# Optimization experiments

Hardware: AMD Instinct MI355X
Metric: run time of the kernel (lower is better)

The kernel has to match this reference:

```python
import jax, jax.numpy as jnp
import numpy as np

EPS = 1e-5  # BatchNorm eps
N_NODES, N_EDGES, F = 100000, 600000, 128


def setup_inputs() -> dict:
    key = jax.random.key(0)
    ks = jax.random.split(key, 16)
    inp = {
        "node_representations": jax.random.normal(ks[0], (N_NODES, F), jnp.float32),
        "edges": jax.random.randint(ks[1], (2, N_EDGES), 0, N_NODES, jnp.int64 if jax.config.jax_enable_x64 else jnp.int32),
        "edge_weights": jax.random.uniform(ks[2], (N_EDGES,), jnp.float32),
        # preprocess FFN: BatchNorm1d(F) [eval mode] + Linear(F, F) + GELU
        "pre_bn_gamma": jax.random.normal(ks[3], (F,), jnp.float32) * 0.1 + 1.0,
        "pre_bn_beta": jax.random.normal(ks[4], (F,), jnp.float32) * 0.1,
        "pre_bn_mean": jax.random.normal(ks[5], (F,), jnp.float32) * 0.1,
        "pre_bn_var": jax.random.uniform(ks[6], (F,), jnp.float32) * 0.5 + 0.5,
        "pre_w": jax.random.normal(ks[7], (F, F), jnp.float32) / np.sqrt(F),
        "pre_b": jnp.zeros((F,), jnp.float32),
        # update FFN: BatchNorm1d(2F) [eval mode] + Linear(2F, F) + GELU
        "upd_bn_gamma": jax.random.normal(ks[8], (2 * F,), jnp.float32) * 0.1 + 1.0,
        "upd_bn_beta": jax.random.normal(ks[9], (2 * F,), jnp.float32) * 0.1,
        "upd_bn_mean": jax.random.normal(ks[10], (2 * F,), jnp.float32) * 0.1,
        "upd_bn_var": jax.random.uniform(ks[11], (2 * F,), jnp.float32) * 0.5 + 0.5,
        "upd_w": jax.random.normal(ks[12], (2 * F, F), jnp.float32) / np.sqrt(2 * F),
        "upd_b": jnp.zeros((F,), jnp.float32),
    }
    return inp


def _bn_eval(x, gamma, beta, mean, var):
    return (x - mean) * (gamma / jnp.sqrt(var + EPS)) + beta


def reference(node_representations, edges, edge_weights,
              pre_bn_gamma, pre_bn_beta, pre_bn_mean, pre_bn_var, pre_w, pre_b,
              upd_bn_gamma, upd_bn_beta, upd_bn_mean, upd_bn_var, upd_w, upd_b):
    n_nodes, f = node_representations.shape
    node_idx, nbr_idx = edges[0], edges[1]
    # gather neighbour features: [E, F]
    x = node_representations[nbr_idx]
    # preprocess FFN (BN eval, dropout=identity in eval, linear, gelu)
    x = _bn_eval(x, pre_bn_gamma, pre_bn_beta, pre_bn_mean, pre_bn_var)
    x = jax.nn.gelu(x @ pre_w + pre_b, approximate=False)
    x = x * edge_weights[:, None]
    # mean aggregation (replicates torch.unique-on-expanded-indices counter = degree * F)
    agg = jax.ops.segment_sum(x, node_idx, num_segments=n_nodes)
    deg = jax.ops.segment_sum(jnp.ones_like(edge_weights), node_idx, num_segments=n_nodes)
    counter = (deg * f)[:, None]
    agg = jnp.where(counter > 0, agg / jnp.where(counter > 0, counter, 1.0), 0.0)
    # concat combine + update FFN
    emb = jnp.concatenate([node_representations, agg], axis=-1)
    emb = _bn_eval(emb, upd_bn_gamma, upd_bn_beta, upd_bn_mean, upd_bn_var)
    emb = jax.nn.gelu(emb @ upd_w + upd_b, approximate=False)
    return emb
```

## Files before the change

kernel.cpp:

```cpp
#include <hip/hip_runtime.h>
#include <math.h>

#define F 128
#define TWO_F 256
#define BN_EPS 1e-5f
#define PAD_W2 264

typedef unsigned short ushort_t;
typedef unsigned char uchar_t;
typedef __attribute__((ext_vector_type(8))) short bfrag;
typedef __attribute__((ext_vector_type(4))) float ffrag;
typedef __attribute__((ext_vector_type(2))) float floatx2;

__device__ __forceinline__ float gelu_exact(float x) {
    return 0.5f * x * (1.0f + erff(x * 0.70710678118654752f));
}
__device__ __forceinline__ ushort_t f2bf(float x) {
    unsigned int u = __float_as_uint(x);
    u = (u + 0x7FFFu + ((u >> 16) & 1u)) >> 16;
    return (ushort_t)u;
}
__device__ __forceinline__ unsigned int pk2(float a, float b) {
    return (unsigned int)f2bf(a) | ((unsigned int)f2bf(b) << 16);
}

__device__ __forceinline__ void fma4_fp8(float* acc, unsigned int d, float w) {
    floatx2 lo = __builtin_amdgcn_cvt_pk_f32_fp8(d, false);
    floatx2 hi = __builtin_amdgcn_cvt_pk_f32_fp8(d, true);
    acc[0] = fmaf(w, lo.x, acc[0]);
    acc[1] = fmaf(w, lo.y, acc[1]);
    acc[2] = fmaf(w, hi.x, acc[2]);
    acc[3] = fmaf(w, hi.y, acc[3]);
}
__device__ __forceinline__ void fma16_fp8(float* acc, uint4 a, float w) {
    fma4_fp8(acc + 0,  a.x, w); fma4_fp8(acc + 4,  a.y, w);
    fma4_fp8(acc + 8,  a.z, w); fma4_fp8(acc + 12, a.w, w);
}

__device__ __forceinline__ bfrag pack8(float4 f0, float4 f1) {
    bfrag a;
    unsigned int* au = reinterpret_cast<unsigned int*>(&a);
    au[0] = pk2(f0.x, f0.y); au[1] = pk2(f0.z, f0.w);
    au[2] = pk2(f1.x, f1.y); au[3] = pk2(f1.z, f1.w);
    return a;
}

__global__ __launch_bounds__(256) void fold_hist(
    const float* __restrict__ pre_w, const float* __restrict__ pre_b,
    const float* __restrict__ g1, const float* __restrict__ be1,
    const float* __restrict__ m1, const float* __restrict__ v1,
    const float* __restrict__ upd_w, const float* __restrict__ upd_b,
    const float* __restrict__ g2, const float* __restrict__ be2,
    const float* __restrict__ m2, const float* __restrict__ v2,
    ushort_t* __restrict__ W1T, ushort_t* __restrict__ W2T,
    float* __restrict__ b1f, float* __restrict__ b2f,
    const int* __restrict__ edges, int* __restrict__ counts,
    int* __restrict__ rankb, int nEdges, int histBlocks) {
    const int t = threadIdx.x;
    if (blockIdx.x == 0) {
        __shared__ float t1[F], t2[TWO_F];
        if (t < F) {
            float s = g1[t] * rsqrtf(v1[t] + BN_EPS);
            t1[t] = be1[t] - m1[t] * s;
        }
        {
            float s = g2[t] * rsqrtf(v2[t] + BN_EPS);
            t2[t] = be2[t] - m2[t] * s;
        }
        __syncthreads();
        if (t < F) {
            float acc = pre_b[t];
            #pragma unroll 16
            for (int k = 0; k < F; ++k) acc = fmaf(t1[k], pre_w[k * F + t], acc);
            b1f[t] = acc;
        } else {
            int j = t - F;
            float acc = upd_b[j];
            #pragma unroll 16
            for (int k = 0; k < TWO_F; ++k) acc = fmaf(t2[k], upd_w[k * F + j], acc);
            b2f[j] = acc;
        }
    } else if (blockIdx.x <= 128) {
        int idx = (blockIdx.x - 1) * 256 + t;
        if (idx < F * F) {
            int k = idx & (F - 1), n = idx >> 7;
            float s = g1[k] * rsqrtf(v1[k] + BN_EPS);
            W1T[idx] = f2bf(s * pre_w[k * F + n]);
        }
        {
            int k = idx & (TWO_F - 1), n = idx >> 8;
            float s = g2[k] * rsqrtf(v2[k] + BN_EPS);
            W2T[idx] = f2bf(s * upd_w[k * F + n]);
        }
    } else {
        int b = blockIdx.x - 129;
        for (int i = b * 256 + t; i < nEdges; i += histBlocks * 256) {
            int rk = atomicAdd(&counts[edges[i]], 1);
            rankb[i] = rk;
        }
    }
}

__global__ __launch_bounds__(1024) void scan_pass1(const int* __restrict__ counts,
                                                   int* __restrict__ offsets,
                                                   int* __restrict__ blocksums, int n) {
    __shared__ int sb[1024];
    const int t = threadIdx.x;
    int idx = blockIdx.x * 1024 + t;
    int v = (idx < n) ? counts[idx] : 0;
    sb[t] = v;
    __syncthreads();
    for (int off = 1; off < 1024; off <<= 1) {
        int x = (t >= off) ? sb[t - off] : 0;
        __syncthreads();
        sb[t] += x;
        __syncthreads();
    }
    if (idx < n) offsets[idx + 1] = sb[t];
    if (t == 1023) blocksums[blockIdx.x] = sb[t];
}

__global__ __launch_bounds__(1024) void scan_pass3(const int* __restrict__ counts,
                                                   int* __restrict__ offsets,
                                                   const int* __restrict__ blocksums,
                                                   int* __restrict__ cursor, int n) {
    __shared__ int sb[1024];
    const int t = threadIdx.x;
    sb[t] = (t < blockIdx.x) ? blocksums[t] : 0;
    __syncthreads();
    #pragma unroll
    for (int off = 512; off > 0; off >>= 1) {
        if (t < off) sb[t] += sb[t + off];
        __syncthreads();
    }
    int base = sb[0];
    int idx = blockIdx.x * 1024 + t;
    if (idx < n) {
        int incl = offsets[idx + 1] + base;
        offsets[idx + 1] = incl;
        cursor[idx] = incl - counts[idx];
    }
    if (blockIdx.x == 0 && t == 0) offsets[0] = 0;
}

__global__ __launch_bounds__(256) void gemm1_fill(
    const float* __restrict__ nodes, const ushort_t* __restrict__ W1T,
    const float* __restrict__ b1f, uchar_t* __restrict__ G8, int nNodes,
    const int* __restrict__ edges, const float* __restrict__ ew,
    const int* __restrict__ offsets, const int* __restrict__ rankb,
    int2* __restrict__ csr, int nEdges, int gemmBlocks, int fillBlocks) {
    const int t = threadIdx.x;

    if (blockIdx.x >= gemmBlocks) {
        int b = blockIdx.x - gemmBlocks;
        for (int e = b * 256 + t; e < nEdges; e += fillBlocks * 256) {
            int dst = edges[e];
            int pos = offsets[dst] + rankb[e];
            csr[pos] = make_int2(edges[nEdges + e], __float_as_int(ew[e]));
        }
        return;
    }

    const int lane = t & 63, w = t >> 6;
    const int m = lane & 15, quad = lane >> 4;
    const int fw = w * 32;

    bfrag wf[2][4];
    #pragma unroll
    for (int cb = 0; cb < 2; ++cb)
        #pragma unroll
        for (int kk = 0; kk < 4; ++kk)
            wf[cb][kk] = *reinterpret_cast<const bfrag*>(
                W1T + (size_t)(fw + cb * 16 + m) * F + kk * 32 + quad * 8);

    float4 bias[2];
    #pragma unroll
    for (int cb = 0; cb < 2; ++cb)
        bias[cb] = *reinterpret_cast<const float4*>(b1f + fw + cb * 16 + quad * 4);

    const int tb = blockIdx.x * 256;

    #pragma unroll 2
    for (int g = 0; g < 16; ++g) {
        const int node = tb + g * 16 + m;
        const int sn = (node < nNodes) ? node : 0;
        const float* np = nodes + (size_t)sn * F + quad * 8;

        bfrag nf[4];
        #pragma unroll
        for (int kk = 0; kk < 4; ++kk) {
            float4 f0 = *reinterpret_cast<const float4*>(np + kk * 32);
            float4 f1 = *reinterpret_cast<const float4*>(np + kk * 32 + 4);
            nf[kk] = pack8(f0, f1);
        }

        ffrag acc[2];
        acc[0] = (ffrag){0.f, 0.f, 0.f, 0.f};
        acc[1] = (ffrag){0.f, 0.f, 0.f, 0.f};
        #pragma unroll
        for (int kk = 0; kk < 4; ++kk) {
            acc[0] = __builtin_amdgcn_mfma_f32_16x16x32_bf16(wf[0][kk], nf[kk], acc[0], 0, 0, 0);
            acc[1] = __builtin_amdgcn_mfma_f32_16x16x32_bf16(wf[1][kk], nf[kk], acc[1], 0, 0, 0);
        }

        if (node < nNodes) {
            #pragma unroll
            for (int cb = 0; cb < 2; ++cb) {
                float v0 = gelu_exact(acc[cb][0] + bias[cb].x);
                float v1 = gelu_exact(acc[cb][1] + bias[cb].y);
                float v2 = gelu_exact(acc[cb][2] + bias[cb].z);
                float v3 = gelu_exact(acc[cb][3] + bias[cb].w);
                int pw = __builtin_amdgcn_cvt_pk_fp8_f32(v0, v1, 0, false);
                pw = __builtin_amdgcn_cvt_pk_fp8_f32(v2, v3, pw, true);
                *reinterpret_cast<unsigned int*>(
                    G8 + (size_t)node * F + fw + cb * 16 + quad * 4) = (unsigned int)pw;
            }
        }
    }
}

__global__ __launch_bounds__(256) void gather_agg(
    const uchar_t* __restrict__ G8, const int* __restrict__ offsets,
    const int2* __restrict__ csr, ushort_t* __restrict__ agg, int nNodes) {
    const int t = threadIdx.x;
    const int gid = blockIdx.x * 32 + (t >> 3);
    const int q = t & 7;
    if (gid >= nNodes) return;
    const int s = offsets[gid], e = offsets[gid + 1];

    float acc[16];
    #pragma unroll
    for (int j = 0; j < 16; ++j) acc[j] = 0.f;

    int i = s;
    while (i < e) {
        int c = e - i;
        c = (c > 8) ? 8 : c;
        uint4 av[8];
        float wv[8];
        #pragma unroll
        for (int j = 0; j < 8; ++j) {
            if (j < c) {
                int2 m = csr[i + j];
                wv[j] = __int_as_float(m.y);
                av[j] = *reinterpret_cast<const uint4*>(
                    G8 + (size_t)(unsigned int)m.x * F + q * 16);
            }
        }
        #pragma unroll
        for (int j = 0; j < 8; ++j)
            if (j < c) fma16_fp8(acc, av[j], wv[j]);
        i += c;
    }

    const int deg = e - s;
    const float inv = (deg > 0) ? 1.0f / ((float)deg * (float)F) : 0.f;
    uint4 pv0, pv1;
    pv0.x = pk2(acc[0] * inv, acc[1] * inv);  pv0.y = pk2(acc[2] * inv, acc[3] * inv);
    pv0.z = pk2(acc[4] * inv, acc[5] * inv);  pv0.w = pk2(acc[6] * inv, acc[7] * inv);
    pv1.x = pk2(acc[8] * inv, acc[9] * inv);  pv1.y = pk2(acc[10] * inv, acc[11] * inv);
    pv1.z = pk2(acc[12] * inv, acc[13] * inv); pv1.w = pk2(acc[14] * inv, acc[15] * inv);
    uint4* d = reinterpret_cast<uint4*>(agg + (size_t)gid * F + q * 16);
    d[0] = pv0; d[1] = pv1;
}

__global__ __launch_bounds__(512, 4) void gemm2(
    const float* __restrict__ nodes, const ushort_t* __restrict__ agg,
    const ushort_t* __restrict__ W2T, const float* __restrict__ b2f,
    float* __restrict__ out, int nNodes) {
    __shared__ ushort_t Wl[F * PAD_W2];
    __shared__ float bsm[F];
    const int t = threadIdx.x;

    for (int j = t; j < 4096; j += 512) {
        int feat = j >> 5, kc = j & 31;
        *reinterpret_cast<uint4*>(Wl + feat * PAD_W2 + kc * 8) =
            reinterpret_cast<const uint4*>(W2T)[j];
    }
    if (t < F) bsm[t] = b2f[t];
    __syncthreads();

    const int lane = t & 63, w = t >> 6;
    const int m = lane & 15, quad = lane >> 4;
    const int tb = blockIdx.x * 256;

    int row0 = tb + w * 32 + m;
    int row1 = row0 + 16;
    int r0c = (row0 < nNodes) ? row0 : 0;
    int r1c = (row1 < nNodes) ? row1 : 0;
    const float*    p0n = nodes + (size_t)r0c * F + quad * 8;
    const float*    p1n = nodes + (size_t)r1c * F + quad * 8;
    const ushort_t* p0a = agg   + (size_t)r0c * F + quad * 8;
    const ushort_t* p1a = agg   + (size_t)r1c * F + quad * 8;

    ffrag acc0[8], acc1[8];
    #pragma unroll
    for (int c = 0; c < 8; ++c) {
        acc0[c] = (ffrag){0.f, 0.f, 0.f, 0.f};
        acc1[c] = (ffrag){0.f, 0.f, 0.f, 0.f};
    }

    #pragma unroll
    for (int kk = 0; kk < 8; ++kk) {
        int k0 = kk * 32 + quad * 8;
        bfrag a0, a1;
        if (kk < 4) {
            float4 f0 = *reinterpret_cast<const float4*>(p0n + kk * 32);
            float4 f1 = *reinterpret_cast<const float4*>(p0n + kk * 32 + 4);
            a0 = pack8(f0, f1);
            float4 g0 = *reinterpret_cast<const float4*>(p1n + kk * 32);
            float4 g1 = *reinterpret_cast<const float4*>(p1n + kk * 32 + 4);
            a1 = pack8(g0, g1);
        } else {
            a0 = *reinterpret_cast<const bfrag*>(p0a + (kk - 4) * 32);
            a1 = *reinterpret_cast<const bfrag*>(p1a + (kk - 4) * 32);
        }
        #pragma unroll
        for (int c = 0; c < 8; ++c) {
            bfrag b = *reinterpret_cast<const bfrag*>(Wl + (c * 16 + m) * PAD_W2 + k0);
            acc0[c] = __builtin_amdgcn_mfma_f32_16x16x32_bf16(a0, b, acc0[c], 0, 0, 0);
            acc1[c] = __builtin_amdgcn_mfma_f32_16x16x32_bf16(a1, b, acc1[c], 0, 0, 0);
        }
    }

    #pragma unroll
    for (int c = 0; c < 8; ++c) {
        int feat = c * 16 + m;
        float bj = bsm[feat];
        #pragma unroll
        for (int i = 0; i < 4; ++i) {
            int n0 = tb + w * 32 + quad * 4 + i;
            if (n0 < nNodes) out[(size_t)n0 * F + feat] = gelu_exact(acc0[c][i] + bj);
            int n1 = n0 + 16;
            if (n1 < nNodes) out[(size_t)n1 * F + feat] = gelu_exact(acc1[c][i] + bj);
        }
    }
}

extern "C" void kernel_launch(void* const* d_in, const int* in_sizes, int n_in,
                              void* d_out, int out_size, void* d_ws, size_t ws_size,
                              hipStream_t stream) {
    const float* nodes  = (const float*)d_in[0];
    const int*   edges  = (const int*)d_in[1];
    const float* ew     = (const float*)d_in[2];
    const float* pre_g  = (const float*)d_in[3];
    const float* pre_be = (const float*)d_in[4];
    const float* pre_m  = (const float*)d_in[5];
    const float* pre_v  = (const float*)d_in[6];
    const float* pre_w  = (const float*)d_in[7];
    const float* pre_b  = (const float*)d_in[8];
    const float* upd_g  = (const float*)d_in[9];
    const float* upd_be = (const float*)d_in[10];
    const float* upd_m  = (const float*)d_in[11];
    const float* upd_v  = (const float*)d_in[12];
    const float* upd_w  = (const float*)d_in[13];
    const float* upd_b  = (const float*)d_in[14];
    float* out = (float*)d_out;

    const int nNodes = in_sizes[0] / F;
    const int nEdges = in_sizes[2];
    const int nChunks = (nNodes + 1023) / 1024;
    const int histBlocks = 1024;
    const int fillBlocks = 512;
    const int gemmBlocks = (nNodes + 255) / 256;

    char* p = (char*)d_ws;
    int*      counts    = (int*)p;       p += (size_t)nNodes * 4;
    int*      offsets   = (int*)p;       p += (size_t)(nNodes + 4) * 4;
    int*      cursor    = (int*)p;       p += (size_t)nNodes * 4;
    int*      blocksums = (int*)p;       p += 1024 * 4;
    int2*     csr       = (int2*)p;      p += (size_t)nEdges * 8;
    float*    b1f       = (float*)p;     p += F * 4;
    float*    b2f       = (float*)p;     p += F * 4;
    ushort_t* W1T       = (ushort_t*)p;  p += F * F * 2;
    ushort_t* W2T       = (ushort_t*)p;  p += TWO_F * F * 2;
    uchar_t*  G8        = (uchar_t*)p;   p += (size_t)nNodes * F;
    ushort_t* agg       = (ushort_t*)p;  p += (size_t)nNodes * F * 2;
    int*      rankb     = (int*)p;

    hipMemsetAsync(counts, 0, (size_t)nNodes * 4, stream);

    fold_hist<<<129 + histBlocks, 256, 0, stream>>>(
        pre_w, pre_b, pre_g, pre_be, pre_m, pre_v,
        upd_w, upd_b, upd_g, upd_be, upd_m, upd_v,
        W1T, W2T, b1f, b2f, edges, counts, rankb, nEdges, histBlocks);

    scan_pass1<<<nChunks, 1024, 0, stream>>>(counts, offsets, blocksums, nNodes);
    scan_pass3<<<nChunks, 1024, 0, stream>>>(counts, offsets, blocksums, cursor, nNodes);

    gemm1_fill<<<gemmBlocks + fillBlocks, 256, 0, stream>>>(
        nodes, W1T, b1f, G8, nNodes, edges, ew, offsets, rankb, csr, nEdges,
        gemmBlocks, fillBlocks);

    gather_agg<<<(nNodes + 31) / 32, 256, 0, stream>>>(
        G8, offsets, csr, agg, nNodes);

    gemm2<<<(nNodes + 255) / 256, 512, 0, stream>>>(
        nodes, agg, W2T, b2f, out, nNodes);
}
```

Baseline: 267.9 us.

## Stage GEMM1 weights in LDS with persistent tiles and vectorize GEMM2 stores

GEMM1 now stages the bf16 weight matrix and bias in shared memory and loops persistently over 64-node tiles. Each wave computes all 128 output features for 16 nodes, so node rows are loaded once per wave and each wave writes full output rows. GEMM2 is restructured so each wave handles 16 nodes across all features and writes float4-vectorized output rows instead of scattered scalar stores. The 4-block occupancy hint on GEMM2 is dropped and its grid uses 128-node blocks. The trade is extra LDS traffic, since weights are reread from shared memory per tile, and higher register use from 8 accumulators.

```diff
diff --git a/kernel.cpp b/kernel.cpp
--- a/kernel.cpp
+++ b/kernel.cpp
@@ -4,6 +4,7 @@
 #define F 128
 #define TWO_F 256
 #define BN_EPS 1e-5f
+#define PAD_W1 136
 #define PAD_W2 264
 
 typedef unsigned short ushort_t;
@@ -148,7 +149,9 @@
     const float* __restrict__ b1f, uchar_t* __restrict__ G8, int nNodes,
     const int* __restrict__ edges, const float* __restrict__ ew,
     const int* __restrict__ offsets, const int* __restrict__ rankb,
-    int2* __restrict__ csr, int nEdges, int gemmBlocks, int fillBlocks) {
+    int2* __restrict__ csr, int nEdges, int gemmBlocks, int fillBlocks, int nTiles) {
+    __shared__ ushort_t Wl[F * PAD_W1];
+    __shared__ float bsm[F];
     const int t = threadIdx.x;
 
     if (blockIdx.x >= gemmBlocks) {
@@ -161,28 +164,19 @@
         return;
     }
 
+    for (int j = t; j < 2048; j += 256) {
+        int feat = j >> 4, kc = j & 15;
+        *reinterpret_cast<uint4*>(Wl + feat * PAD_W1 + kc * 8) =
+            reinterpret_cast<const uint4*>(W1T)[j];
+    }
+    if (t < F) bsm[t] = b1f[t];
+    __syncthreads();
+
     const int lane = t & 63, w = t >> 6;
     const int m = lane & 15, quad = lane >> 4;
-    const int fw = w * 32;
-
-    bfrag wf[2][4];
-    #pragma unroll
-    for (int cb = 0; cb < 2; ++cb)
-        #pragma unroll
-        for (int kk = 0; kk < 4; ++kk)
-            wf[cb][kk] = *reinterpret_cast<const bfrag*>(
-                W1T + (size_t)(fw + cb * 16 + m) * F + kk * 32 + quad * 8);
-
-    float4 bias[2];
-    #pragma unroll
-    for (int cb = 0; cb < 2; ++cb)
-        bias[cb] = *reinterpret_cast<const float4*>(b1f + fw + cb * 16 + quad * 4);
-
-    const int tb = blockIdx.x * 256;
-
-    #pragma unroll 2
-    for (int g = 0; g < 16; ++g) {
-        const int node = tb + g * 16 + m;
+
+    for (int tile = blockIdx.x; tile < nTiles; tile += gemmBlocks) {
+        const int node = tile * 64 + w * 16 + m;
         const int sn = (node < nNodes) ? node : 0;
         const float* np = nodes + (size_t)sn * F + quad * 8;
 
@@ -194,26 +188,32 @@
             nf[kk] = pack8(f0, f1);
         }
 
-        ffrag acc[2];
-        acc[0] = (ffrag){0.f, 0.f, 0.f, 0.f};
-        acc[1] = (ffrag){0.f, 0.f, 0.f, 0.f};
+        ffrag acc[8];
+        #pragma unroll
+        for (int cb = 0; cb < 8; ++cb) acc[cb] = (ffrag){0.f, 0.f, 0.f, 0.f};
+
         #pragma unroll
         for (int kk = 0; kk < 4; ++kk) {
-            acc[0] = __builtin_amdgcn_mfma_f32_16x16x32_bf16(wf[0][kk], nf[kk], acc[0], 0, 0, 0);
-            acc[1] = __builtin_amdgcn_mfma_f32_16x16x32_bf16(wf[1][kk], nf[kk], acc[1], 0, 0, 0);
+            int ko = kk * 32 + quad * 8;
+            #pragma unroll
+            for (int cb = 0; cb < 8; ++cb) {
+                bfrag a = *reinterpret_cast<const bfrag*>(Wl + (cb * 16 + m) * PAD_W1 + ko);
+                acc[cb] = __builtin_amdgcn_mfma_f32_16x16x32_bf16(a, nf[kk], acc[cb], 0, 0, 0);
+            }
         }
 
         if (node < nNodes) {
             #pragma unroll
-            for (int cb = 0; cb < 2; ++cb) {
-                float v0 = gelu_exact(acc[cb][0] + bias[cb].x);
-                float v1 = gelu_exact(acc[cb][1] + bias[cb].y);
-                float v2 = gelu_exact(acc[cb][2] + bias[cb].z);
-                float v3 = gelu_exact(acc[cb][3] + bias[cb].w);
+            for (int cb = 0; cb < 8; ++cb) {
+                float4 bj = *reinterpret_cast<const float4*>(bsm + cb * 16 + quad * 4);
+                float v0 = gelu_exact(acc[cb][0] + bj.x);
+                float v1 = gelu_exact(acc[cb][1] + bj.y);
+                float v2 = gelu_exact(acc[cb][2] + bj.z);
+                float v3 = gelu_exact(acc[cb][3] + bj.w);
                 int pw = __builtin_amdgcn_cvt_pk_fp8_f32(v0, v1, 0, false);
                 pw = __builtin_amdgcn_cvt_pk_fp8_f32(v2, v3, pw, true);
                 *reinterpret_cast<unsigned int*>(
-                    G8 + (size_t)node * F + fw + cb * 16 + quad * 4) = (unsigned int)pw;
+                    G8 + (size_t)node * F + cb * 16 + quad * 4) = (unsigned int)pw;
             }
         }
     }
@@ -264,7 +264,7 @@
     d[0] = pv0; d[1] = pv1;
 }
 
-__global__ __launch_bounds__(512, 4) void gemm2(
+__global__ __launch_bounds__(512) void gemm2(
     const float* __restrict__ nodes, const ushort_t* __restrict__ agg,
     const ushort_t* __restrict__ W2T, const float* __restrict__ b2f,
     float* __restrict__ out, int nNodes) {
@@ -282,57 +282,47 @@
 
     const int lane = t & 63, w = t >> 6;
     const int m = lane & 15, quad = lane >> 4;
-    const int tb = blockIdx.x * 256;
-
-    int row0 = tb + w * 32 + m;
-    int row1 = row0 + 16;
-    int r0c = (row0 < nNodes) ? row0 : 0;
-    int r1c = (row1 < nNodes) ? row1 : 0;
-    const float*    p0n = nodes + (size_t)r0c * F + quad * 8;
-    const float*    p1n = nodes + (size_t)r1c * F + quad * 8;
-    const ushort_t* p0a = agg   + (size_t)r0c * F + quad * 8;
-    const ushort_t* p1a = agg   + (size_t)r1c * F + quad * 8;
-
-    ffrag acc0[8], acc1[8];
-    #pragma unroll
-    for (int c = 0; c < 8; ++c) {
-        acc0[c] = (ffrag){0.f, 0.f, 0.f, 0.f};
-        acc1[c] = (ffrag){0.f, 0.f, 0.f, 0.f};
-    }
+
+    const int node = blockIdx.x * 128 + w * 16 + m;
+    const int sn = (node < nNodes) ? node : 0;
+    const float*    np = nodes + (size_t)sn * F + quad * 8;
+    const ushort_t* pa = agg   + (size_t)sn * F + quad * 8;
+
+    bfrag nf[8];
+    #pragma unroll
+    for (int kk = 0; kk < 4; ++kk) {
+        float4 f0 = *reinterpret_cast<const float4*>(np + kk * 32);
+        float4 f1 = *reinterpret_cast<const float4*>(np + kk * 32 + 4);
+        nf[kk] = pack8(f0, f1);
+    }
+    #pragma unroll
+    for (int kk = 4; kk < 8; ++kk)
+        nf[kk] = *reinterpret_cast<const bfrag*>(pa + (kk - 4) * 32);
+
+    ffrag acc[8];
+    #pragma unroll
+    for (int cb = 0; cb < 8; ++cb) acc[cb] = (ffrag){0.f, 0.f, 0.f, 0.f};
 
     #pragma unroll
     for (int kk = 0; kk < 8; ++kk) {
-        int k0 = kk * 32 + quad * 8;
-        bfrag a0, a1;
-        if (kk < 4) {
-            float4 f0 = *reinterpret_cast<const float4*>(p0n + kk * 32);
-            float4 f1 = *reinterpret_cast<const float4*>(p0n + kk * 32 + 4);
-            a0 = pack8(f0, f1);
-            float4 g0 = *reinterpret_cast<const float4*>(p1n + kk * 32);
-            float4 g1 = *reinterpret_cast<const float4*>(p1n + kk * 32 + 4);
-            a1 = pack8(g0, g1);
-        } else {
-            a0 = *reinterpret_cast<const bfrag*>(p0a + (kk - 4) * 32);
-            a1 = *reinterpret_cast<const bfrag*>(p1a + (kk - 4) * 32);
-        }
-        #pragma unroll
-        for (int c = 0; c < 8; ++c) {
-            bfrag b = *reinterpret_cast<const bfrag*>(Wl + (c * 16 + m) * PAD_W2 + k0);
-            acc0[c] = __builtin_amdgcn_mfma_f32_16x16x32_bf16(a0, b, acc0[c], 0, 0, 0);
-            acc1[c] = __builtin_amdgcn_mfma_f32_16x16x32_bf16(a1, b, acc1[c], 0, 0, 0);
-        }
-    }
-
-    #pragma unroll
-    for (int c = 0; c < 8; ++c) {
-        int feat = c * 16 + m;
-        float bj = bsm[feat];
-        #pragma unroll
-        for (int i = 0; i < 4; ++i) {
-            int n0 = tb + w * 32 + quad * 4 + i;
-            if (n0 < nNodes) out[(size_t)n0 * F + feat] = gelu_exact(acc0[c][i] + bj);
-            int n1 = n0 + 16;
-            if (n1 < nNodes) out[(size_t)n1 * F + feat] = gelu_exact(acc1[c][i] + bj);
+        int ko = kk * 32 + quad * 8;
+        #pragma unroll
+        for (int cb = 0; cb < 8; ++cb) {
+            bfrag a = *reinterpret_cast<const bfrag*>(Wl + (cb * 16 + m) * PAD_W2 + ko);
+            acc[cb] = __builtin_amdgcn_mfma_f32_16x16x32_bf16(a, nf[kk], acc[cb], 0, 0, 0);
+        }
+    }
+
+    if (node < nNodes) {
+        #pragma unroll
+        for (int cb = 0; cb < 8; ++cb) {
+            float4 bj = *reinterpret_cast<const float4*>(bsm + cb * 16 + quad * 4);
+            float4 o;
+            o.x = gelu_exact(acc[cb][0] + bj.x);
+            o.y = gelu_exact(acc[cb][1] + bj.y);
+            o.z = gelu_exact(acc[cb][2] + bj.z);
+            o.w = gelu_exact(acc[cb][3] + bj.w);
+            *reinterpret_cast<float4*>(out + (size_t)node * F + cb * 16 + quad * 4) = o;
         }
     }
 }
@@ -362,7 +352,8 @@
     const int nChunks = (nNodes + 1023) / 1024;
     const int histBlocks = 1024;
     const int fillBlocks = 512;
-    const int gemmBlocks = (nNodes + 255) / 256;
+    const int nTiles = (nNodes + 63) / 64;
+    const int gemmBlocks = (nTiles < 1024) ? nTiles : 1024;
 
     char* p = (char*)d_ws;
     int*      counts    = (int*)p;       p += (size_t)nNodes * 4;
@@ -390,11 +381,11 @@
 
     gemm1_fill<<<gemmBlocks + fillBlocks, 256, 0, stream>>>(
         nodes, W1T, b1f, G8, nNodes, edges, ew, offsets, rankb, csr, nEdges,
-        gemmBlocks, fillBlocks);
+        gemmBlocks, fillBlocks, nTiles);
 
     gather_agg<<<(nNodes + 31) / 32, 256, 0, stream>>>(
         G8, offsets, csr, agg, nNodes);
 
-    gemm2<<<(nNodes + 255) / 256, 512, 0, stream>>>(
+    gemm2<<<(nNodes + 127) / 128, 512, 0, stream>>>(
         nodes, agg, W2T, b2f, out, nNodes);
 }
```

Result: faster. 250.3 us (-6.6%).
